# Optimization experiments

Measured on AMD Instinct MI355X. Metric: run time of the kernel, lower is better.

Reference implementation:

```python
import jax, jax.numpy as jnp
import numpy as np

H, HS, C = 16, 64, 1024  # num_heads, head_size, n_embd

def setup_inputs() -> dict:
    key = jax.random.key(0)
    ks = jax.random.split(key, 5)
    B, T = 2, 2048
    s = 1.0 / np.sqrt(C)
    return {
        "x": jax.random.normal(ks[0], (B, T, C), dtype=jnp.float32),
        "Wq": jax.random.normal(ks[1], (H, C, HS), dtype=jnp.float32) * s,
        "Wk": jax.random.normal(ks[2], (H, C, HS), dtype=jnp.float32) * s,
        "Wv": jax.random.normal(ks[3], (H, C, HS), dtype=jnp.float32) * s,
        "Wo": jax.random.normal(ks[4], (C, C), dtype=jnp.float32) * s,
    }

def reference(x, Wq, Wk, Wv, Wo):
    B, T, Cdim = x.shape
    scale = Cdim ** -0.5  # original scales by n_embd**-0.5, not head_size
    q = jnp.einsum('btc,hcd->bhtd', x, Wq)
    k = jnp.einsum('btc,hcd->bhtd', x, Wk)
    v = jnp.einsum('btc,hcd->bhtd', x, Wv)
    wei = jnp.einsum('bhtd,bhsd->bhts', q, k) * scale  # [B,H,T,T]
    causal = jnp.tril(jnp.ones((T, T), dtype=bool))
    wei = jnp.where(causal, wei, -jnp.inf)
    wei = jax.nn.softmax(wei, axis=-1)
    out = jnp.einsum('bhts,bhsd->bhtd', wei, v)  # [B,H,T,HS]
    out = out.transpose(0, 2, 1, 3).reshape(B, T, -1)  # concat heads -> [B,T,C]
    return out @ Wo.T
```

## Files before the change

kernel.cpp:

```cpp
#include <hip/hip_runtime.h>

typedef unsigned short ushort_t;
typedef __bf16 bf16x8 __attribute__((ext_vector_type(8)));
typedef float f32x4 __attribute__((ext_vector_type(4)));
typedef float f32x16 __attribute__((ext_vector_type(16)));
typedef unsigned short ushortx8 __attribute__((ext_vector_type(8)));
typedef unsigned int uintx4 __attribute__((ext_vector_type(4)));

#define NH 16
#define HS 64
#define CD 1024
#define NB 2
#define NT 2048
#define BT (NB * NT)
#define N3 (3 * CD)

#define L2E_DIV32 0.04508422002778011f

#define QKV_LD 2048
#define PART1_OFF 50331648
#define SLOT_BYTES 18432
#define WAVE_BYTES 4608
#define R0_SLOTS 796


__device__ __forceinline__ ushort_t bf16_rne(float f) {
  union { float f; unsigned u; } v; v.f = f;
  unsigned u = v.u;
  unsigned r = (u + 0x7FFFu + ((u >> 16) & 1u)) >> 16;
  return (ushort_t)r;
}

__device__ __forceinline__ float bf2f(ushort_t u) {
  union { unsigned u; float f; } v; v.u = ((unsigned)u) << 16; return v.f;
}

__device__ __forceinline__ void gload_lds16(const ushort_t* g, ushort_t* l) {
  __builtin_amdgcn_global_load_lds(
      (const __attribute__((address_space(1))) unsigned int*)g,
      (__attribute__((address_space(3))) unsigned int*)l, 16, 0, 0);
}

__device__ __forceinline__ f32x4 mfma16(ushortx8 a, ushortx8 b, f32x4 c) {
  return __builtin_amdgcn_mfma_f32_16x16x32_bf16(
      __builtin_bit_cast(bf16x8, a), __builtin_bit_cast(bf16x8, b), c, 0, 0, 0);
}

__device__ __forceinline__ f32x16 mfma32(ushortx8 a, ushortx8 b, f32x16 c) {
  return __builtin_amdgcn_mfma_f32_32x32x16_bf16(
      __builtin_bit_cast(bf16x8, a), __builtin_bit_cast(bf16x8, b), c, 0, 0, 0);
}

__device__ __forceinline__ unsigned cvt_pk_bf16(float lo, float hi) {
  unsigned r;
  asm("v_cvt_pk_bf16_f32 %0, %1, %2" : "=v"(r) : "v"(lo), "v"(hi));
  return r;
}

__device__ __forceinline__ void plswap(unsigned &a, unsigned &b) {
  asm volatile("v_permlane32_swap_b32 %0, %1" : "+v"(a), "+v"(b));
}


__global__ __launch_bounds__(256)
void pack_cast(const float4* __restrict__ in, ushort_t* __restrict__ out, int n4) {
  const int i = blockIdx.x * 256 + threadIdx.x;
  if (i >= n4) return;
  const float4 v = in[i];
  ushort4 r;
  r.x = bf16_rne(v.x); r.y = bf16_rne(v.y);
  r.z = bf16_rne(v.z); r.w = bf16_rne(v.w);
  *(ushort4*)(out + (size_t)i * 4) = r;
}

__global__ __launch_bounds__(256)
void pack_wqkv(const float* __restrict__ Wq, const float* __restrict__ Wk,
               const float* __restrict__ Wv, ushort_t* __restrict__ out) {
  __shared__ ushort_t tile[64 * 66];
  const int sh = blockIdx.y;
  const int s = sh >> 4, h = sh & 15;
  const float* W = (s == 0) ? Wq : ((s == 1) ? Wk : Wv);
  const int c0 = blockIdx.x * 64;
  const int t = threadIdx.x;
#pragma unroll
  for (int j = 0; j < 16; ++j) {
    const int idx = t + j * 256;
    const int ci = idx >> 6, d = idx & 63;
    const float v = W[(size_t)(h * 1024 + c0 + ci) * 64 + d];
    tile[d * 66 + ci] = bf16_rne(v);
  }
  __syncthreads();
#pragma unroll
  for (int j = 0; j < 16; ++j) {
    const int idx = t + j * 256;
    const int d = idx >> 6, ci = idx & 63;
    out[(size_t)(s * 1024 + h * 64 + d) * 1024 + c0 + ci] = tile[d * 66 + ci];
  }
}


template <int MODE>
__global__ __launch_bounds__(256)
void gemm_bt(const ushort_t* __restrict__ A, const ushort_t* __restrict__ Bt,
             void* __restrict__ Cv, ushort_t* __restrict__ Vt,
             int M, int N, int K) {
  __shared__ __align__(16) ushort_t ldsA[2][128 * 32];
  __shared__ __align__(16) ushort_t ldsB[2][128 * 32];
  const int tid = threadIdx.x;
  const int lane = tid & 63;
  const int wave = tid >> 6;
  const int row0 = blockIdx.y * 128;
  const int col0 = blockIdx.x * 128;
  const int wm = wave >> 1, wn = wave & 1;

  f32x4 acc[4][4] = {};

  const int ce = (tid & 3) * 8;

  auto stage = [&](int buf, int kt) {
    const int kbase = kt * 32;
#pragma unroll
    for (int j = 0; j < 2; ++j) {
      const int r = j * 64 + (tid >> 2);
      gload_lds16(A + (size_t)(row0 + r) * K + kbase + ce,
                  &ldsA[buf][(j * 256 + wave * 64) * 8]);
      gload_lds16(Bt + (size_t)(col0 + r) * K + kbase + ce,
                  &ldsB[buf][(j * 256 + wave * 64) * 8]);
    }
  };

  const int arow_off = (wm * 64 + (lane & 15)) * 32 + (lane >> 4) * 8;
  const int brow_off = (wn * 64 + (lane & 15)) * 32 + (lane >> 4) * 8;

  auto compute = [&](int buf) {
    ushortx8 af[4], bfr[4];
#pragma unroll
    for (int m = 0; m < 4; ++m)
      af[m] = *(const ushortx8*)&ldsA[buf][arow_off + m * 512];
#pragma unroll
    for (int n = 0; n < 4; ++n)
      bfr[n] = *(const ushortx8*)&ldsB[buf][brow_off + n * 512];
#pragma unroll
    for (int m = 0; m < 4; ++m)
#pragma unroll
      for (int n = 0; n < 4; ++n)
        acc[m][n] = mfma16(af[m], bfr[n], acc[m][n]);
  };

  stage(0, 0);
  __syncthreads();
  const int nk = K >> 5;
  for (int kt = 0; kt < nk; ++kt) {
    const int cur = kt & 1;
    if (kt + 1 < nk) stage(cur ^ 1, kt + 1);
    compute(cur);
    __syncthreads();
  }

#pragma unroll
  for (int m = 0; m < 4; ++m) {
    const int rbase = row0 + wm * 64 + m * 16 + (lane >> 4) * 4;
#pragma unroll
    for (int n = 0; n < 4; ++n) {
      const int col = col0 + wn * 64 + n * 16 + (lane & 15);
      if constexpr (MODE == 0) {
#pragma unroll
        for (int i = 0; i < 4; ++i)
          ((float*)Cv)[(size_t)(rbase + i) * N + col] = acc[m][n][i];
      } else {
        if (col < 2048) {
          const float sc = (col < 1024) ? L2E_DIV32 : 1.0f;
#pragma unroll
          for (int i = 0; i < 4; ++i)
            ((ushort_t*)Cv)[(size_t)(rbase + i) * QKV_LD + col] =
                bf16_rne(acc[m][n][i] * sc);
        } else {
          const int dcol = col - 2048;
          const int bI = rbase >> 11;
          const int t0i = rbase & 2047;
          ushort4 pk;
          pk.x = bf16_rne(acc[m][n][0]);
          pk.y = bf16_rne(acc[m][n][1]);
          pk.z = bf16_rne(acc[m][n][2]);
          pk.w = bf16_rne(acc[m][n][3]);
          *(ushort4*)(Vt + (size_t)(bI * 1024 + dcol) * NT + t0i) = pk;
        }
      }
    }
  }
}


__global__ __launch_bounds__(256, 3)
void attn_fwd7(const ushort_t* __restrict__ QKV, const ushort_t* __restrict__ Vt,
               ushort_t* __restrict__ O, char* __restrict__ wsb) {
  __shared__ __align__(16) ushort_t Klds[2][64 * 64];
  __shared__ __align__(16) ushort_t Vlds[2][64 * 64];

  const int tid = threadIdx.x;
  const int lane = tid & 63;
  const int w = tid >> 6;
  const int l31 = lane & 31;
  const int h = lane >> 5;

  const int x = blockIdx.x;
  const int bh = x & 31;
  const int c = x >> 5;
  int qb, j, k;
  if (c < 16)      { qb = 12 + (c >> 2); j = c & 3; k = 4; }
  else if (c < 28) { const int e = c - 16; const int q = e / 3; qb = 8 + q; j = e - q * 3; k = 3; }
  else if (c < 36) { const int e = c - 28; qb = 4 + (e >> 1); j = e & 1; k = 2; }
  else             { qb = c - 36; j = 0; k = 1; }
  const int nt = 2 * qb + 2;
  const int bsz = nt / k, rem = nt - bsz * k;
  const int t0 = j * bsz + (j < rem ? j : rem);
  const int t1 = t0 + bsz + (j < rem ? 1 : 0);
  const bool lastc = (t1 == nt);

  const int b = bh >> 4, head = bh & 15;
  const size_t base = (size_t)b * NT * QKV_LD;
  const int qg = qb * 128 + w * 32 + l31;
  const int tmax = lastc ? (2 * qb + (w >> 1)) : (t1 - 1);

  ushortx8 qf[4];
  {
    const ushort_t* qp = QKV + base + (size_t)qg * QKV_LD + head * 64 + h * 8;
#pragma unroll
    for (int kc = 0; kc < 4; ++kc) qf[kc] = *(const ushortx8*)(qp + kc * 16);
  }
  asm volatile("s_waitcnt vmcnt(0)" ::: "memory");

  int koff[4];
#pragma unroll
  for (int kc = 0; kc < 4; ++kc)
    koff[kc] = l31 * 128 + (((2 * kc + h) ^ (l31 & 7)) * 16);

  const int rowA = tid >> 3, ccA = tid & 7;
  const int rowB = 32 + rowA;
  const ushort_t* kg = QKV + base + 1024 + head * 64;
  const ushort_t* vg = Vt + (size_t)(bh * 64) * NT;
  const ushort_t* ksA = kg + (size_t)(t0 * 64 + rowA) * QKV_LD + ((ccA ^ (rowA & 7)) * 8);
  const ushort_t* ksB = kg + (size_t)(t0 * 64 + rowB) * QKV_LD + ((ccA ^ (rowB & 7)) * 8);
  const ushort_t* vsA = vg + (size_t)rowA * NT + t0 * 64 + ((ccA ^ (rowA & 7)) * 8);
  const ushort_t* vsB = vg + (size_t)rowB * NT + t0 * 64 + ((ccA ^ (rowB & 7)) * 8);
  const size_t kadv = (size_t)64 * QKV_LD;

  f32x16 oA = {}, oB = {};
  float m_r = -INFINITY, l_r = 0.f;

  gload_lds16(ksA, &Klds[0][(w * 64) * 8]);
  gload_lds16(ksB, &Klds[0][(256 + w * 64) * 8]);
  gload_lds16(vsA, &Vlds[0][(w * 64) * 8]);
  gload_lds16(vsB, &Vlds[0][(256 + w * 64) * 8]);

  int curb = 0;
  for (int t = t0; t < t1; ++t) {
    const bool hasn = (t + 1 < t1);
    const int nxt = curb ^ 1;
    if (hasn) {
      ksA += kadv; ksB += kadv; vsA += 64; vsB += 64;
      gload_lds16(ksA, &Klds[nxt][(w * 64) * 8]);
      gload_lds16(ksB, &Klds[nxt][(256 + w * 64) * 8]);
      gload_lds16(vsA, &Vlds[nxt][(w * 64) * 8]);
      gload_lds16(vsB, &Vlds[nxt][(256 + w * 64) * 8]);
      asm volatile("s_waitcnt vmcnt(4)" ::: "memory");
    } else {
      asm volatile("s_waitcnt vmcnt(0)" ::: "memory");
    }
    __builtin_amdgcn_s_barrier();
    asm volatile("" ::: "memory");

    if (t <= tmax) {
      const bool diag = lastc && (t == tmax);
      const bool halfB = diag && ((w & 1) == 0);
      const char* kb = (const char*)&Klds[curb][0];
      const char* vb = (const char*)&Vlds[curb][0];

      f32x16 sA = {}, sB = {};
#pragma unroll
      for (int kc = 0; kc < 4; ++kc)
        sA = mfma32(*(const ushortx8*)(kb + koff[kc]), qf[kc], sA);
      if (!halfB) {
#pragma unroll
        for (int kc = 0; kc < 4; ++kc)
          sB = mfma32(*(const ushortx8*)(kb + 4096 + koff[kc]), qf[kc], sB);
      }

      if (diag) {
#pragma unroll
        for (int r = 0; r < 16; ++r) {
          const int krow = (r & 3) + 8 * (r >> 2) + 4 * h;
          if (halfB) { if (krow > l31) sA[r] = -INFINITY; }
          else       { if (krow > l31) sB[r] = -INFINITY; }
        }
      }

      float mm[16];
#pragma unroll
      for (int r = 0; r < 16; ++r) mm[r] = halfB ? sA[r] : fmaxf(sA[r], sB[r]);
#pragma unroll
      for (int st = 8; st >= 1; st >>= 1)
#pragma unroll
        for (int r = 0; r < st; ++r) mm[r] = fmaxf(mm[r], mm[r + st]);
      const float mx = fmaxf(mm[0], __shfl_xor(mm[0], 32, 64));

      if (__any(mx > m_r + 8.0f)) {
        const float mn = fmaxf(m_r, mx);
        const float al = exp2f(m_r - mn);
        m_r = mn; l_r *= al;
#pragma unroll
        for (int r = 0; r < 16; ++r) { oA[r] *= al; oB[r] *= al; }
      }

      unsigned u[16];
      float ps[8];
#pragma unroll
      for (int jj = 0; jj < 8; ++jj) {
        const float e0 = exp2f(sA[2 * jj] - m_r);
        const float e1 = exp2f(sA[2 * jj + 1] - m_r);
        u[jj] = cvt_pk_bf16(e0, e1);
        ps[jj] = e0 + e1;
      }
      if (!halfB) {
#pragma unroll
        for (int jj = 0; jj < 8; ++jj) {
          const float e0 = exp2f(sB[2 * jj] - m_r);
          const float e1 = exp2f(sB[2 * jj + 1] - m_r);
          u[8 + jj] = cvt_pk_bf16(e0, e1);
          ps[jj] += e0 + e1;
        }
      }
#pragma unroll
      for (int st = 4; st >= 1; st >>= 1)
#pragma unroll
        for (int r = 0; r < st; ++r) ps[r] += ps[r + st];
      l_r += ps[0] + __shfl_xor(ps[0], 32, 64);

      plswap(u[0], u[2]);   plswap(u[1], u[3]);
      plswap(u[4], u[6]);   plswap(u[5], u[7]);
      if (!halfB) {
        plswap(u[8], u[10]);  plswap(u[9], u[11]);
        plswap(u[12], u[14]); plswap(u[13], u[15]);
      }

#pragma unroll
      for (int kc = 0; kc < 4; ++kc) {
        if (kc < 2 || !halfB) {
          uintx4 pw;
          pw[0] = u[4 * kc + 0]; pw[1] = u[4 * kc + 1];
          pw[2] = u[4 * kc + 2]; pw[3] = u[4 * kc + 3];
          const ushortx8 pav = __builtin_bit_cast(ushortx8, pw);
          oA = mfma32(*(const ushortx8*)(vb + koff[kc]), pav, oA);
          oB = mfma32(*(const ushortx8*)(vb + 4096 + koff[kc]), pav, oB);
        }
      }
    }

    __builtin_amdgcn_s_barrier();
    asm volatile("" ::: "memory");
    curb ^= 1;
  }

  if (k == 1) {
    const float inv_l = 1.0f / l_r;
    ushort_t* op = O + ((size_t)(b * NT + qg)) * 1024 + head * 64;
#pragma unroll
    for (int db = 0; db < 2; ++db)
#pragma unroll
      for (int g = 0; g < 4; ++g) {
        ushort4 pk;
        pk.x = bf16_rne((db ? oB[4 * g + 0] : oA[4 * g + 0]) * inv_l);
        pk.y = bf16_rne((db ? oB[4 * g + 1] : oA[4 * g + 1]) * inv_l);
        pk.z = bf16_rne((db ? oB[4 * g + 2] : oA[4 * g + 2]) * inv_l);
        pk.w = bf16_rne((db ? oB[4 * g + 3] : oA[4 * g + 3]) * inv_l);
        *(ushort4*)(op + db * 32 + 8 * g + 4 * h) = pk;
      }
  } else {
    const int local = (qb < 8) ? ((qb - 4) * 2 + j)
                    : (qb < 12) ? (8 + (qb - 8) * 3 + j)
                    : (20 + (qb - 12) * 4 + j);
    const int s = bh * 36 + local;
    char* wb = (s < R0_SLOTS ? wsb + (size_t)s * SLOT_BYTES
                             : wsb + PART1_OFF + (size_t)(s - R0_SLOTS) * SLOT_BYTES)
               + w * WAVE_BYTES;
#pragma unroll
    for (int g = 0; g < 4; ++g) {
      ushortx8 pk;
#pragma unroll
      for (int e2 = 0; e2 < 8; ++e2)
        pk[e2] = bf16_rne(g < 2 ? oA[g * 8 + e2] : oB[(g - 2) * 8 + e2]);
      *(ushortx8*)(wb + lane * 64 + g * 16) = pk;
    }
    *(float*)(wb + 4096 + lane * 4) = m_r;
    *(float*)(wb + 4352 + lane * 4) = l_r;
  }
}

__global__ __launch_bounds__(256)
void attn_merge(const char* __restrict__ wsb, ushort_t* __restrict__ O) {
  const int x = blockIdx.x;
  const int bh = x & 31;
  const int qi = x >> 5;
  const int qb = 4 + qi;
  const int k  = qi < 4 ? 2 : (qi < 8 ? 3 : 4);
  const int lb = qi < 4 ? qi * 2 : (qi < 8 ? 8 + (qi - 4) * 3 : 20 + (qi - 8) * 4);
  const int tid = threadIdx.x;
  const int lane = tid & 63;
  const int w = tid >> 6;
  const int l31 = lane & 31;
  const int h = lane >> 5;

  const char* wbs[4];
  float mj[4], lj[4];
  float M = -INFINITY;
#pragma unroll
  for (int jj = 0; jj < 4; ++jj) {
    if (jj < k) {
      const int s = bh * 36 + lb + jj;
      const char* wb = (s < R0_SLOTS ? wsb + (size_t)s * SLOT_BYTES
                                     : wsb + PART1_OFF + (size_t)(s - R0_SLOTS) * SLOT_BYTES)
                       + w * WAVE_BYTES;
      wbs[jj] = wb;
      mj[jj] = *(const float*)(wb + 4096 + lane * 4);
      lj[jj] = *(const float*)(wb + 4352 + lane * 4);
      M = fmaxf(M, mj[jj]);
    }
  }
  float o[32];
#pragma unroll
  for (int r = 0; r < 32; ++r) o[r] = 0.f;
  float lacc = 0.f;
#pragma unroll
  for (int jj = 0; jj < 4; ++jj) {
    if (jj < k) {
      const float a = exp2f(mj[jj] - M);
      lacc += a * lj[jj];
#pragma unroll
      for (int g = 0; g < 4; ++g) {
        const ushortx8 v = *(const ushortx8*)(wbs[jj] + lane * 64 + g * 16);
#pragma unroll
        for (int e = 0; e < 8; ++e) o[g * 8 + e] += a * bf2f(v[e]);
      }
    }
  }
  const float inv_l = 1.0f / lacc;
  const int b = bh >> 4, head = bh & 15;
  const int qg = qb * 128 + w * 32 + l31;
  ushort_t* op = O + ((size_t)(b * NT + qg)) * 1024 + head * 64;
#pragma unroll
  for (int db = 0; db < 2; ++db)
#pragma unroll
    for (int g = 0; g < 4; ++g) {
      ushort4 pk;
      pk.x = bf16_rne(o[db * 16 + 4 * g + 0] * inv_l);
      pk.y = bf16_rne(o[db * 16 + 4 * g + 1] * inv_l);
      pk.z = bf16_rne(o[db * 16 + 4 * g + 2] * inv_l);
      pk.w = bf16_rne(o[db * 16 + 4 * g + 3] * inv_l);
      *(ushort4*)(op + db * 32 + 8 * g + 4 * h) = pk;
    }
}


extern "C" void kernel_launch(void* const* d_in, const int* in_sizes, int n_in,
                              void* d_out, int out_size, void* d_ws, size_t ws_size,
                              hipStream_t stream) {
  (void)in_sizes; (void)n_in; (void)out_size; (void)ws_size;
  const float* x  = (const float*)d_in[0];
  const float* Wq = (const float*)d_in[1];
  const float* Wk = (const float*)d_in[2];
  const float* Wv = (const float*)d_in[3];
  const float* Wo = (const float*)d_in[4];

  char* ws = (char*)d_ws;
  ushort_t* Xbf    = (ushort_t*)(ws);
  ushort_t* Wqkv_t = (ushort_t*)(ws + 8388608);
  ushort_t* Wo_bf  = (ushort_t*)(ws + 14680064);
  ushort_t* QKV    = (ushort_t*)(ws + 16777216);
  ushort_t* Vt     = (ushort_t*)(ws + 33554432);
  ushort_t* Obf    = (ushort_t*)(ws + 41943040);

  pack_cast<<<4096, 256, 0, stream>>>((const float4*)x, Xbf, 1048576);
  pack_cast<<<1024, 256, 0, stream>>>((const float4*)Wo, Wo_bf, 262144);
  pack_wqkv<<<dim3(16, 48), 256, 0, stream>>>(Wq, Wk, Wv, Wqkv_t);

  gemm_bt<1><<<dim3(24, 32), 256, 0, stream>>>(Xbf, Wqkv_t, QKV, Vt, BT, N3, CD);
  attn_fwd7<<<1280, 256, 0, stream>>>(QKV, Vt, Obf, ws);
  attn_merge<<<384, 256, 0, stream>>>(ws, Obf);
  gemm_bt<0><<<dim3(8, 32), 256, 0, stream>>>(Obf, Wo_bf, d_out, nullptr, BT, CD, CD);
}
```

Measured before the change: 132.9 us.

## Rebalance attention split-KV chunks, triple-buffer K/V and drop trailing barrier

```diff
diff --git a/kernel.cpp b/kernel.cpp
--- a/kernel.cpp
+++ b/kernel.cpp
@@ -18,10 +18,32 @@
 #define L2E_DIV32 0.04508422002778011f
 
 #define QKV_LD 2048
-#define PART1_OFF 50331648
 #define SLOT_BYTES 18432
 #define WAVE_BYTES 4608
 #define R0_SLOTS 796
+
+__constant__ static const int QB_TAB[51] = {
+  0,1,2, 3,3, 4,4, 5,5, 6,6,6, 7,7,7, 8,8,8,
+  9,9,9,9, 10,10,10,10, 11,11,11,11,
+  12,12,12,12,12, 13,13,13,13,13, 14,14,14,14,14,
+  15,15,15,15,15,15};
+__constant__ static const int K_TAB[51] = {
+  1,1,1, 2,2, 2,2, 2,2, 3,3,3, 3,3,3, 3,3,3,
+  4,4,4,4, 4,4,4,4, 4,4,4,4,
+  5,5,5,5,5, 5,5,5,5,5, 5,5,5,5,5,
+  6,6,6,6,6,6};
+__constant__ static const int T0_TAB[51] = {
+  0, 0, 0, 0,4, 0,5, 0,6, 0,5,10, 0,6,11, 0,6,12,
+  0,5,10,15, 0,6,12,17, 0,6,12,18,
+  0,6,11,16,21, 0,6,12,18,23, 0,6,12,18,24,
+  0,6,12,17,22,27};
+__constant__ static const int T1_TAB[51] = {
+  2, 4, 6, 4,8, 5,10, 6,12, 5,10,14, 6,11,16, 6,12,18,
+  5,10,15,20, 6,12,17,22, 6,12,18,24,
+  6,11,16,21,26, 6,12,18,23,28, 6,12,18,24,30,
+  6,12,17,22,27,32};
+__constant__ static const int FIRSTC_TAB[16] = {
+  0,1,2,3,5,7,9,12,15,18,22,26,30,35,40,45};
 
 
 __device__ __forceinline__ ushort_t bf16_rne(float f) {
@@ -59,6 +81,11 @@
 
 __device__ __forceinline__ void plswap(unsigned &a, unsigned &b) {
   asm volatile("v_permlane32_swap_b32 %0, %1" : "+v"(a), "+v"(b));
+}
+
+__device__ __forceinline__ const char* slot_ptr(const char* wsb, const char* dout, int s) {
+  return (s < R0_SLOTS) ? wsb + (size_t)s * SLOT_BYTES
+                        : dout + (size_t)(s - R0_SLOTS) * SLOT_BYTES;
 }
 
 
@@ -192,10 +219,10 @@
 
 
 __global__ __launch_bounds__(256, 3)
-void attn_fwd7(const ushort_t* __restrict__ QKV, const ushort_t* __restrict__ Vt,
-               ushort_t* __restrict__ O, char* __restrict__ wsb) {
-  __shared__ __align__(16) ushort_t Klds[2][64 * 64];
-  __shared__ __align__(16) ushort_t Vlds[2][64 * 64];
+void attn_fwd8(const ushort_t* __restrict__ QKV, const ushort_t* __restrict__ Vt,
+               ushort_t* __restrict__ O, char* __restrict__ wsb,
+               char* __restrict__ dout) {
+  __shared__ __align__(16) ushort_t KV[3][2][4096];
 
   const int tid = threadIdx.x;
   const int lane = tid & 63;
@@ -205,16 +232,12 @@
 
   const int x = blockIdx.x;
   const int bh = x & 31;
-  const int c = x >> 5;
-  int qb, j, k;
-  if (c < 16)      { qb = 12 + (c >> 2); j = c & 3; k = 4; }
-  else if (c < 28) { const int e = c - 16; const int q = e / 3; qb = 8 + q; j = e - q * 3; k = 3; }
-  else if (c < 36) { const int e = c - 28; qb = 4 + (e >> 1); j = e & 1; k = 2; }
-  else             { qb = c - 36; j = 0; k = 1; }
+  const int c = 50 - (x >> 5);
+  const int qb = QB_TAB[c];
+  const int k  = K_TAB[c];
+  const int t0 = T0_TAB[c];
+  const int t1 = T1_TAB[c];
   const int nt = 2 * qb + 2;
-  const int bsz = nt / k, rem = nt - bsz * k;
-  const int t0 = j * bsz + (j < rem ? j : rem);
-  const int t1 = t0 + bsz + (j < rem ? 1 : 0);
   const bool lastc = (t1 == nt);
 
   const int b = bh >> 4, head = bh & 15;
@@ -248,21 +271,20 @@
   f32x16 oA = {}, oB = {};
   float m_r = -INFINITY, l_r = 0.f;
 
-  gload_lds16(ksA, &Klds[0][(w * 64) * 8]);
-  gload_lds16(ksB, &Klds[0][(256 + w * 64) * 8]);
-  gload_lds16(vsA, &Vlds[0][(w * 64) * 8]);
-  gload_lds16(vsB, &Vlds[0][(256 + w * 64) * 8]);
-
-  int curb = 0;
+  gload_lds16(ksA, &KV[0][0][w * 512]);
+  gload_lds16(ksB, &KV[0][0][2048 + w * 512]);
+  gload_lds16(vsA, &KV[0][1][w * 512]);
+  gload_lds16(vsB, &KV[0][1][2048 + w * 512]);
+
+  int cur = 0;
   for (int t = t0; t < t1; ++t) {
-    const bool hasn = (t + 1 < t1);
-    const int nxt = curb ^ 1;
-    if (hasn) {
+    int nxt = cur + 1; if (nxt == 3) nxt = 0;
+    if (t + 1 < t1) {
       ksA += kadv; ksB += kadv; vsA += 64; vsB += 64;
-      gload_lds16(ksA, &Klds[nxt][(w * 64) * 8]);
-      gload_lds16(ksB, &Klds[nxt][(256 + w * 64) * 8]);
-      gload_lds16(vsA, &Vlds[nxt][(w * 64) * 8]);
-      gload_lds16(vsB, &Vlds[nxt][(256 + w * 64) * 8]);
+      gload_lds16(ksA, &KV[nxt][0][w * 512]);
+      gload_lds16(ksB, &KV[nxt][0][2048 + w * 512]);
+      gload_lds16(vsA, &KV[nxt][1][w * 512]);
+      gload_lds16(vsB, &KV[nxt][1][2048 + w * 512]);
       asm volatile("s_waitcnt vmcnt(4)" ::: "memory");
     } else {
       asm volatile("s_waitcnt vmcnt(0)" ::: "memory");
@@ -273,8 +295,8 @@
     if (t <= tmax) {
       const bool diag = lastc && (t == tmax);
       const bool halfB = diag && ((w & 1) == 0);
-      const char* kb = (const char*)&Klds[curb][0];
-      const char* vb = (const char*)&Vlds[curb][0];
+      const char* kb = (const char*)&KV[cur][0][0];
+      const char* vb = (const char*)&KV[cur][1][0];
 
       f32x16 sA = {}, sB = {};
 #pragma unroll
@@ -356,9 +378,7 @@
       }
     }
 
-    __builtin_amdgcn_s_barrier();
-    asm volatile("" ::: "memory");
-    curb ^= 1;
+    cur = nxt;
   }
 
   if (k == 1) {
@@ -376,13 +396,8 @@
         *(ushort4*)(op + db * 32 + 8 * g + 4 * h) = pk;
       }
   } else {
-    const int local = (qb < 8) ? ((qb - 4) * 2 + j)
-                    : (qb < 12) ? (8 + (qb - 8) * 3 + j)
-                    : (20 + (qb - 12) * 4 + j);
-    const int s = bh * 36 + local;
-    char* wb = (s < R0_SLOTS ? wsb + (size_t)s * SLOT_BYTES
-                             : wsb + PART1_OFF + (size_t)(s - R0_SLOTS) * SLOT_BYTES)
-               + w * WAVE_BYTES;
+    const int s = bh * 51 + c;
+    char* wb = (char*)slot_ptr(wsb, dout, s) + w * WAVE_BYTES;
 #pragma unroll
     for (int g = 0; g < 4; ++g) {
       ushortx8 pk;
@@ -397,50 +412,38 @@
 }
 
 __global__ __launch_bounds__(256)
-void attn_merge(const char* __restrict__ wsb, ushort_t* __restrict__ O) {
+void attn_merge(const char* __restrict__ wsb, const char* __restrict__ dout,
+                ushort_t* __restrict__ O) {
   const int x = blockIdx.x;
   const int bh = x & 31;
-  const int qi = x >> 5;
-  const int qb = 4 + qi;
-  const int k  = qi < 4 ? 2 : (qi < 8 ? 3 : 4);
-  const int lb = qi < 4 ? qi * 2 : (qi < 8 ? 8 + (qi - 4) * 3 : 20 + (qi - 8) * 4);
+  const int qb = 3 + (x >> 5);
+  const int f = FIRSTC_TAB[qb];
+  const int k = K_TAB[f];
   const int tid = threadIdx.x;
   const int lane = tid & 63;
   const int w = tid >> 6;
   const int l31 = lane & 31;
   const int h = lane >> 5;
-
-  const char* wbs[4];
-  float mj[4], lj[4];
+  const int sbase = bh * 51 + f;
+
   float M = -INFINITY;
-#pragma unroll
-  for (int jj = 0; jj < 4; ++jj) {
-    if (jj < k) {
-      const int s = bh * 36 + lb + jj;
-      const char* wb = (s < R0_SLOTS ? wsb + (size_t)s * SLOT_BYTES
-                                     : wsb + PART1_OFF + (size_t)(s - R0_SLOTS) * SLOT_BYTES)
-                       + w * WAVE_BYTES;
-      wbs[jj] = wb;
-      mj[jj] = *(const float*)(wb + 4096 + lane * 4);
-      lj[jj] = *(const float*)(wb + 4352 + lane * 4);
-      M = fmaxf(M, mj[jj]);
-    }
+  for (int jj = 0; jj < k; ++jj) {
+    const char* wb = slot_ptr(wsb, dout, sbase + jj) + w * WAVE_BYTES;
+    M = fmaxf(M, *(const float*)(wb + 4096 + lane * 4));
   }
   float o[32];
 #pragma unroll
   for (int r = 0; r < 32; ++r) o[r] = 0.f;
   float lacc = 0.f;
-#pragma unroll
-  for (int jj = 0; jj < 4; ++jj) {
-    if (jj < k) {
-      const float a = exp2f(mj[jj] - M);
-      lacc += a * lj[jj];
-#pragma unroll
-      for (int g = 0; g < 4; ++g) {
-        const ushortx8 v = *(const ushortx8*)(wbs[jj] + lane * 64 + g * 16);
-#pragma unroll
-        for (int e = 0; e < 8; ++e) o[g * 8 + e] += a * bf2f(v[e]);
-      }
+  for (int jj = 0; jj < k; ++jj) {
+    const char* wb = slot_ptr(wsb, dout, sbase + jj) + w * WAVE_BYTES;
+    const float a = exp2f(*(const float*)(wb + 4096 + lane * 4) - M);
+    lacc += a * *(const float*)(wb + 4352 + lane * 4);
+#pragma unroll
+    for (int g = 0; g < 4; ++g) {
+      const ushortx8 v = *(const ushortx8*)(wb + lane * 64 + g * 16);
+#pragma unroll
+      for (int e = 0; e < 8; ++e) o[g * 8 + e] += a * bf2f(v[e]);
     }
   }
   const float inv_l = 1.0f / lacc;
@@ -484,7 +487,7 @@
   pack_wqkv<<<dim3(16, 48), 256, 0, stream>>>(Wq, Wk, Wv, Wqkv_t);
 
   gemm_bt<1><<<dim3(24, 32), 256, 0, stream>>>(Xbf, Wqkv_t, QKV, Vt, BT, N3, CD);
-  attn_fwd7<<<1280, 256, 0, stream>>>(QKV, Vt, Obf, ws);
-  attn_merge<<<384, 256, 0, stream>>>(ws, Obf);
+  attn_fwd8<<<1632, 256, 0, stream>>>(QKV, Vt, Obf, ws, (char*)d_out);
+  attn_merge<<<416, 256, 0, stream>>>(ws, (char*)d_out, Obf);
   gemm_bt<0><<<dim3(8, 32), 256, 0, stream>>>(Obf, Wo_bf, d_out, nullptr, BT, CD, CD);
 }
```

After: 133.5 us. Within noise of the previous version (+0.4%).
